# Kernel tuning notes

Hardware: AMD Instinct MI355X
Metric: run time of the kernel (lower is better)

The kernel has to match this reference:

```python
import jax, jax.numpy as jnp
import numpy as np

NEG_BIG = -9e15  # matches torch's -9000000000000000.0 mask value
LEAKY_SLOPE = 0.2  # alpha passed to nn.LeakyReLU


def setup_inputs() -> dict:
    key = jax.random.key(0)
    k1, k2, k3, k4, k5 = jax.random.split(key, 5)
    N, din, de, dout = 500, 100, 200, 100
    return {
        "input_relations": jax.random.normal(k1, (N, din), dtype=jnp.float32),
        "input_entity_embeds": jax.random.normal(k2, (N, N, de), dtype=jnp.float32),
        "relation_adj": jax.random.randint(k3, (N, N), 0, 2, dtype=jnp.int32),
        "a": jax.random.normal(k4, (dout, 2 * din + de), dtype=jnp.float32) * 0.05,
        "a_2": jax.random.normal(k5, (1, dout), dtype=jnp.float32) * 0.05,
    }


def reference(input_relations, input_entity_embeds, relation_adj, a, a_2):
    # Faithful to: a_input[k=(i,j)] = concat(rel_i, rel_j, ent[i,j]); e = a @ a_input
    # We avoid materializing the (N*N, 2*din+de) concat by splitting `a` into the
    # three blocks that hit rel_i, rel_j and ent[i,j] respectively.
    N, din = input_relations.shape
    de = input_entity_embeds.shape[-1]
    a_src = a[:, :din]          # (dout, din) acts on rel_i
    a_dst = a[:, din:2 * din]   # (dout, din) acts on rel_j
    a_ent = a[:, 2 * din:]      # (dout, de)  acts on ent[i,j]

    # e[i, j, o] = a @ concat(rel_i, rel_j, ent_ij)   -> (N, N, dout)
    e = (
        (input_relations @ a_src.T)[:, None, :]
        + (input_relations @ a_dst.T)[None, :, :]
        + jnp.einsum("ijd,od->ijo", input_entity_embeds.reshape(N, N, de), a_ent)
    )

    # scalar score per pair, leaky relu, masked softmax over neighbors j (dim=1)
    e2 = jax.nn.leaky_relu(e @ a_2[0], LEAKY_SLOPE)  # (N, N)
    scores = jnp.where(relation_adj > 0, e2, jnp.float32(NEG_BIG))
    attention = jax.nn.softmax(scores, axis=1)  # (N, N)

    # weighted sum of the score features e (note: original multiplies attention by e,
    # the pre-leakyrelu linear scores, not by a transformed h)
    h_prime = jnp.einsum("ij,ijo->io", attention, e)  # (N, dout)
    return jax.nn.elu(h_prime)  # concat=True branch
```

## Files before the change

kernel.cpp:

```cpp
#include <hip/hip_runtime.h>
#include <stdint.h>
#include <math.h>

#define N     500
#define DIN   100
#define DE    200
#define DOUT  100
#define AROW  (2*DIN + DE)
#define SLOPE 0.2f

#define JCH   8
#define CROWS 63
#define KP    512
#define BK    720
#define DEP   208

typedef __attribute__((ext_vector_type(8)))  short short8;
typedef __attribute__((ext_vector_type(16))) float f32x16;

static __device__ __forceinline__ unsigned short f2bf(float f) {
  union { float f; uint32_t u; } v; v.f = f;
  uint32_t r = (v.u + 0x7FFFu + ((v.u >> 16) & 1u)) >> 16;
  return (unsigned short)r;
}

__global__ __launch_bounds__(256)
void setup_kernel(const float* __restrict__ R, const float* __restrict__ A,
                  const float* __restrict__ a2,
                  float* __restrict__ src, float* __restrict__ ssrc,
                  float* __restrict__ sdst, float* __restrict__ wv,
                  unsigned short* __restrict__ Bcat, unsigned short* __restrict__ Pbuf) {
  int b = blockIdx.x, t = threadIdx.x;
  if (b < N) {
    int i = b;
    __shared__ float rrow[DIN];
    __shared__ float sred[4];
    if (t < DIN) rrow[t] = R[i * DIN + t];
    if (t < KP - N) Pbuf[i * KP + N + t] = 0;
    __syncthreads();
    int o = -1; bool isSrc = false;
    if (t < DOUT) { o = t; isSrc = true; }
    else if (t >= 128 && t < 128 + DOUT) { o = t - 128; }
    float val = 0.f;
    if (o >= 0) {
      const float* arow = A + o * AROW + (isSrc ? 0 : DIN);
      #pragma unroll 4
      for (int d = 0; d < DIN; ++d) val += rrow[d] * arow[d];
      if (isSrc) src[i * DOUT + o] = val;
      else       Bcat[o * BK + i] = f2bf(val);
    }
    float red = (o >= 0) ? val * a2[o] : 0.f;
    #pragma unroll
    for (int k = 1; k < 64; k <<= 1) red += __shfl_xor(red, k, 64);
    if ((t & 63) == 0) sred[t >> 6] = red;
    __syncthreads();
    if (t == 0)   ssrc[i] = sred[0] + sred[1];
    if (t == 128) sdst[i] = sred[2] + sred[3];
  } else if (b == N) {
    if (t < DE) {
      float s = 0.f;
      for (int o = 0; o < DOUT; ++o) s += A[o * AROW + 2 * DIN + t] * a2[o];
      wv[t] = s;
    }
  } else {
    int o = b - (N + 1);
    if (t < DE) Bcat[o * BK + KP + t] = f2bf(A[o * AROW + 2 * DIN + t]);
    if (t < KP - N) Bcat[o * BK + N + t] = 0;
    if (t >= 32 && t < 32 + (BK - KP - DE)) Bcat[o * BK + KP + DE + (t - 32)] = 0;
  }
}

__global__ __launch_bounds__(128)
void passA(const float* __restrict__ E, const int* __restrict__ adj,
           const float* __restrict__ ssrcA, const float* __restrict__ sdstA,
           const float* __restrict__ wv,
           unsigned short* __restrict__ Pbuf,
           float* __restrict__ gws, float* __restrict__ Zws) {
  int bid = blockIdx.x;
  int i = bid >> 3, c = bid & 7;
  int jbeg = c * CROWS;
  int jend = jbeg + CROWS; if (jend > N) jend = N;
  int t = threadIdx.x, wid = t >> 6, lane = t & 63;

  float4 w4 = make_float4(0.f, 0.f, 0.f, 0.f);
  if (lane < 50) w4 = *(const float4*)(wv + lane * 4);

  float4 g = make_float4(0.f, 0.f, 0.f, 0.f);
  float Z = 0.f;
  float ssrc_i = ssrcA[i];
  const float* Erow = E + (size_t)i * N * DE;
  const int* adjrow = adj + (size_t)i * N;

  int j = jbeg + wid;
  for (; j + 2 < jend; j += 4) {
    int a0 = adjrow[j], a1 = adjrow[j + 2];
    float4 ev0 = make_float4(0.f, 0.f, 0.f, 0.f);
    float4 ev1 = make_float4(0.f, 0.f, 0.f, 0.f);
    if (a0 > 0 && lane < 50) ev0 = *(const float4*)(Erow + (size_t)j * DE + lane * 4);
    if (a1 > 0 && lane < 50) ev1 = *(const float4*)(Erow + (size_t)(j + 2) * DE + lane * 4);
    float d0 = ev0.x * w4.x + ev0.y * w4.y + ev0.z * w4.z + ev0.w * w4.w;
    float d1 = ev1.x * w4.x + ev1.y * w4.y + ev1.z * w4.z + ev1.w * w4.w;
    #pragma unroll
    for (int k = 1; k < 64; k <<= 1) { d0 += __shfl_xor(d0, k, 64); d1 += __shfl_xor(d1, k, 64); }
    float p0 = 0.f, p1 = 0.f;
    if (a0 > 0) {
      float e2 = ssrc_i + sdstA[j] + d0;
      e2 = e2 > 0.f ? e2 : SLOPE * e2;
      p0 = __expf(e2); Z += p0;
      g.x += p0 * ev0.x; g.y += p0 * ev0.y; g.z += p0 * ev0.z; g.w += p0 * ev0.w;
    }
    if (a1 > 0) {
      float e2 = ssrc_i + sdstA[j + 2] + d1;
      e2 = e2 > 0.f ? e2 : SLOPE * e2;
      p1 = __expf(e2); Z += p1;
      g.x += p1 * ev1.x; g.y += p1 * ev1.y; g.z += p1 * ev1.z; g.w += p1 * ev1.w;
    }
    if (lane == 0) { Pbuf[i * KP + j] = f2bf(p0); Pbuf[i * KP + j + 2] = f2bf(p1); }
  }
  for (; j < jend; j += 2) {
    int a0 = adjrow[j];
    float4 ev0 = make_float4(0.f, 0.f, 0.f, 0.f);
    float p0 = 0.f;
    if (a0 > 0) {
      if (lane < 50) ev0 = *(const float4*)(Erow + (size_t)j * DE + lane * 4);
      float d0 = ev0.x * w4.x + ev0.y * w4.y + ev0.z * w4.z + ev0.w * w4.w;
      #pragma unroll
      for (int k = 1; k < 64; k <<= 1) d0 += __shfl_xor(d0, k, 64);
      float e2 = ssrc_i + sdstA[j] + d0;
      e2 = e2 > 0.f ? e2 : SLOPE * e2;
      p0 = __expf(e2); Z += p0;
      g.x += p0 * ev0.x; g.y += p0 * ev0.y; g.z += p0 * ev0.z; g.w += p0 * ev0.w;
    }
    if (lane == 0) Pbuf[i * KP + j] = f2bf(p0);
  }

  __shared__ float gl[2][200];
  __shared__ float zl[2];
  if (lane < 50) *(float4*)&gl[wid][lane * 4] = g;
  if (lane == 0) zl[wid] = Z;
  __syncthreads();
  if (wid == 0) {
    if (lane < 50) {
      float4 a = *(float4*)&gl[0][lane * 4];
      float4 b = *(float4*)&gl[1][lane * 4];
      *(float4*)(gws + (size_t)(i * JCH + c) * DE + lane * 4) =
          make_float4(a.x + b.x, a.y + b.y, a.z + b.z, a.w + b.w);
    }
    if (lane == 0) Zws[i * JCH + c] = zl[0] + zl[1];
  }
}

__global__ __launch_bounds__(64)
void gsum_kernel(const float* __restrict__ gws, const float* __restrict__ Zws,
                 unsigned short* __restrict__ gsum, float* __restrict__ Zsum) {
  int i = blockIdx.x, t = threadIdx.x;
  if (t < 50) {
    float4 s = make_float4(0.f, 0.f, 0.f, 0.f);
    #pragma unroll
    for (int c = 0; c < JCH; ++c) {
      float4 v = *(const float4*)(gws + (size_t)(i * JCH + c) * DE + t * 4);
      s.x += v.x; s.y += v.y; s.z += v.z; s.w += v.w;
    }
    ushort4 pk; pk.x = f2bf(s.x); pk.y = f2bf(s.y); pk.z = f2bf(s.z); pk.w = f2bf(s.w);
    *(ushort4*)(gsum + (size_t)i * DEP + t * 4) = pk;
  } else if (t == 50) {
    ushort4 z = {0, 0, 0, 0};
    *(ushort4*)(gsum + (size_t)i * DEP + 200) = z;
    *(ushort4*)(gsum + (size_t)i * DEP + 204) = z;
  } else if (t == 51) {
    float z = 0.f;
    #pragma unroll
    for (int c = 0; c < JCH; ++c) z += Zws[i * JCH + c];
    Zsum[i] = z;
  }
}

__global__ __launch_bounds__(256)
void combine_kernel(const float* __restrict__ src,
                    const unsigned short* __restrict__ Pbuf,
                    const unsigned short* __restrict__ Bcat,
                    const unsigned short* __restrict__ gsum,
                    const float* __restrict__ Zsum,
                    float* __restrict__ out) {
  int b = blockIdx.x;
  int t = threadIdx.x;
  int i0 = b * 32;
  int wave = t >> 6, lane = t & 63, c31 = lane & 31, hi = lane >> 5;
  int o = wave * 32 + c31;
  int arow = i0 + c31; if (arow > N - 1) arow = N - 1;

  const unsigned short* Prow = Pbuf + (size_t)arow * KP;
  const unsigned short* grow = gsum + (size_t)arow * DEP;

  f32x16 acc = {};
  #pragma unroll
  for (int ks = 0; ks < 45; ++ks) {
    short8 a, bf;
    if (ks < 32) a = *(const short8*)(Prow + ks * 16 + hi * 8);
    else         a = *(const short8*)(grow + (ks - 32) * 16 + hi * 8);
    if (o < DOUT) bf = *(const short8*)(Bcat + (size_t)o * BK + ks * 16 + hi * 8);
    else { short8 zz = {}; bf = zz; }
    acc = __builtin_amdgcn_mfma_f32_32x32x16_bf16(a, bf, acc, 0, 0, 0);
  }

  if (o < DOUT) {
    #pragma unroll
    for (int r = 0; r < 16; ++r) {
      int row = (r & 3) + 8 * (r >> 2) + 4 * hi;
      int i = i0 + row;
      if (i < N) {
        float h = src[i * DOUT + o] + acc[r] / Zsum[i];
        out[i * DOUT + o] = h > 0.f ? h : expm1f(h);
      }
    }
  }
}

extern "C" void kernel_launch(void* const* d_in, const int* in_sizes, int n_in,
                              void* d_out, int out_size, void* d_ws, size_t ws_size,
                              hipStream_t stream) {
  const float* R   = (const float*)d_in[0];
  const float* E   = (const float*)d_in[1];
  const int*   adj = (const int*)d_in[2];
  const float* A   = (const float*)d_in[3];
  const float* a2  = (const float*)d_in[4];
  float* out = (float*)d_out;

  char* wsb = (char*)d_ws;
  float*          src  = (float*)(wsb + 0);
  float*          ssrc = (float*)(wsb + 200000);
  float*          sdst = (float*)(wsb + 202000);
  float*          wv   = (float*)(wsb + 204000);
  unsigned short* Bcat = (unsigned short*)(wsb + 204800);
  unsigned short* Pbuf = (unsigned short*)(wsb + 348800);
  float*          gws  = (float*)(wsb + 860800);
  float*          Zws  = (float*)(wsb + 4060800);
  unsigned short* gsum = (unsigned short*)(wsb + 4076800);
  float*          Zsum = (float*)(wsb + 4284800);

  setup_kernel<<<N + 1 + DOUT, 256, 0, stream>>>(R, A, a2, src, ssrc, sdst, wv, Bcat, Pbuf);
  passA<<<N * JCH, 128, 0, stream>>>(E, adj, ssrc, sdst, wv, Pbuf, gws, Zws);
  gsum_kernel<<<N, 64, 0, stream>>>(gws, Zws, gsum, Zsum);
  combine_kernel<<<16, 256, 0, stream>>>(src, Pbuf, Bcat, gsum, Zsum, out);
}
```

Baseline: 64.38 us.

## Compact active neighbors per chunk and reduce partials with atomics, dropping gsum kernel

Measured after the change: 57.53 us. 10.6% less time.

```diff
diff --git a/kernel.cpp b/kernel.cpp
--- a/kernel.cpp
+++ b/kernel.cpp
@@ -9,11 +9,12 @@
 #define AROW  (2*DIN + DE)
 #define SLOPE 0.2f
 
-#define JCH   8
-#define CROWS 63
+#define JCH   4
+#define CROWS 125
 #define KP    512
 #define BK    720
 #define DEP   208
+#define GZF   104000
 
 typedef __attribute__((ext_vector_type(8)))  short short8;
 typedef __attribute__((ext_vector_type(16))) float f32x16;
@@ -29,7 +30,8 @@
                   const float* __restrict__ a2,
                   float* __restrict__ src, float* __restrict__ ssrc,
                   float* __restrict__ sdst, float* __restrict__ wv,
-                  unsigned short* __restrict__ Bcat, unsigned short* __restrict__ Pbuf) {
+                  unsigned short* __restrict__ Bcat, unsigned short* __restrict__ Pbuf,
+                  float* __restrict__ gsum, float* __restrict__ Zsum) {
   int b = blockIdx.x, t = threadIdx.x;
   if (b < N) {
     int i = b;
@@ -62,124 +64,121 @@
       for (int o = 0; o < DOUT; ++o) s += A[o * AROW + 2 * DIN + t] * a2[o];
       wv[t] = s;
     }
-  } else {
+  } else if (b <= N + DOUT) {
     int o = b - (N + 1);
     if (t < DE) Bcat[o * BK + KP + t] = f2bf(A[o * AROW + 2 * DIN + t]);
     if (t < KP - N) Bcat[o * BK + N + t] = 0;
     if (t >= 32 && t < 32 + (BK - KP - DE)) Bcat[o * BK + KP + DE + (t - 32)] = 0;
-  }
-}
-
-__global__ __launch_bounds__(128)
+  } else if (b <= 702) {
+    int off = (b - 601) * 1024 + t * 4;
+    if (off < GZF) *(float4*)(gsum + off) = make_float4(0.f, 0.f, 0.f, 0.f);
+  } else {
+    if (t < 125) *(float4*)(Zsum + t * 4) = make_float4(0.f, 0.f, 0.f, 0.f);
+  }
+}
+
+__global__ __launch_bounds__(256)
 void passA(const float* __restrict__ E, const int* __restrict__ adj,
            const float* __restrict__ ssrcA, const float* __restrict__ sdstA,
            const float* __restrict__ wv,
            unsigned short* __restrict__ Pbuf,
-           float* __restrict__ gws, float* __restrict__ Zws) {
+           float* __restrict__ gsum, float* __restrict__ Zsum) {
+  __shared__ int list[128];
+  __shared__ int cntS;
+  __shared__ float gl[4][200];
+  __shared__ float zl[4];
+
   int bid = blockIdx.x;
-  int i = bid >> 3, c = bid & 7;
+  int i = bid >> 2, c = bid & 3;
   int jbeg = c * CROWS;
-  int jend = jbeg + CROWS; if (jend > N) jend = N;
   int t = threadIdx.x, wid = t >> 6, lane = t & 63;
+
+  if (t == 0) cntS = 0;
+  __syncthreads();
+
+  bool active = false;
+  if (t < CROWS) active = (adj[(size_t)i * N + jbeg + t] > 0);
+  unsigned long long mask = __ballot(active);
+  int wbase = 0;
+  if (lane == 0 && mask) wbase = atomicAdd(&cntS, __popcll(mask));
+  wbase = __shfl(wbase, 0);
+  if (active) {
+    list[wbase + __popcll(mask & ((1ull << lane) - 1ull))] = jbeg + t;
+  } else if (t < CROWS) {
+    Pbuf[i * KP + jbeg + t] = 0;
+  }
+  __syncthreads();
+  int cnt = cntS;
 
   float4 w4 = make_float4(0.f, 0.f, 0.f, 0.f);
   if (lane < 50) w4 = *(const float4*)(wv + lane * 4);
-
   float4 g = make_float4(0.f, 0.f, 0.f, 0.f);
   float Z = 0.f;
   float ssrc_i = ssrcA[i];
   const float* Erow = E + (size_t)i * N * DE;
-  const int* adjrow = adj + (size_t)i * N;
-
-  int j = jbeg + wid;
-  for (; j + 2 < jend; j += 4) {
-    int a0 = adjrow[j], a1 = adjrow[j + 2];
-    float4 ev0 = make_float4(0.f, 0.f, 0.f, 0.f);
-    float4 ev1 = make_float4(0.f, 0.f, 0.f, 0.f);
-    if (a0 > 0 && lane < 50) ev0 = *(const float4*)(Erow + (size_t)j * DE + lane * 4);
-    if (a1 > 0 && lane < 50) ev1 = *(const float4*)(Erow + (size_t)(j + 2) * DE + lane * 4);
-    float d0 = ev0.x * w4.x + ev0.y * w4.y + ev0.z * w4.z + ev0.w * w4.w;
-    float d1 = ev1.x * w4.x + ev1.y * w4.y + ev1.z * w4.z + ev1.w * w4.w;
-    #pragma unroll
-    for (int k = 1; k < 64; k <<= 1) { d0 += __shfl_xor(d0, k, 64); d1 += __shfl_xor(d1, k, 64); }
-    float p0 = 0.f, p1 = 0.f;
-    if (a0 > 0) {
-      float e2 = ssrc_i + sdstA[j] + d0;
-      e2 = e2 > 0.f ? e2 : SLOPE * e2;
-      p0 = __expf(e2); Z += p0;
-      g.x += p0 * ev0.x; g.y += p0 * ev0.y; g.z += p0 * ev0.z; g.w += p0 * ev0.w;
-    }
-    if (a1 > 0) {
-      float e2 = ssrc_i + sdstA[j + 2] + d1;
-      e2 = e2 > 0.f ? e2 : SLOPE * e2;
-      p1 = __expf(e2); Z += p1;
-      g.x += p1 * ev1.x; g.y += p1 * ev1.y; g.z += p1 * ev1.z; g.w += p1 * ev1.w;
-    }
-    if (lane == 0) { Pbuf[i * KP + j] = f2bf(p0); Pbuf[i * KP + j + 2] = f2bf(p1); }
-  }
-  for (; j < jend; j += 2) {
-    int a0 = adjrow[j];
-    float4 ev0 = make_float4(0.f, 0.f, 0.f, 0.f);
-    float p0 = 0.f;
-    if (a0 > 0) {
-      if (lane < 50) ev0 = *(const float4*)(Erow + (size_t)j * DE + lane * 4);
-      float d0 = ev0.x * w4.x + ev0.y * w4.y + ev0.z * w4.z + ev0.w * w4.w;
-      #pragma unroll
-      for (int k = 1; k < 64; k <<= 1) d0 += __shfl_xor(d0, k, 64);
-      float e2 = ssrc_i + sdstA[j] + d0;
-      e2 = e2 > 0.f ? e2 : SLOPE * e2;
-      p0 = __expf(e2); Z += p0;
-      g.x += p0 * ev0.x; g.y += p0 * ev0.y; g.z += p0 * ev0.z; g.w += p0 * ev0.w;
-    }
-    if (lane == 0) Pbuf[i * KP + j] = f2bf(p0);
-  }
-
-  __shared__ float gl[2][200];
-  __shared__ float zl[2];
+
+  for (int base = wid * 4; base + 3 < cnt; base += 16) {
+    int j0 = list[base], j1 = list[base + 1], j2 = list[base + 2], j3 = list[base + 3];
+    float4 e0 = make_float4(0.f,0.f,0.f,0.f), e1 = e0, e2v = e0, e3 = e0;
+    if (lane < 50) {
+      e0  = *(const float4*)(Erow + (size_t)j0 * DE + lane * 4);
+      e1  = *(const float4*)(Erow + (size_t)j1 * DE + lane * 4);
+      e2v = *(const float4*)(Erow + (size_t)j2 * DE + lane * 4);
+      e3  = *(const float4*)(Erow + (size_t)j3 * DE + lane * 4);
+    }
+    float d0 = e0.x*w4.x + e0.y*w4.y + e0.z*w4.z + e0.w*w4.w;
+    float d1 = e1.x*w4.x + e1.y*w4.y + e1.z*w4.z + e1.w*w4.w;
+    float d2 = e2v.x*w4.x + e2v.y*w4.y + e2v.z*w4.z + e2v.w*w4.w;
+    float d3 = e3.x*w4.x + e3.y*w4.y + e3.z*w4.z + e3.w*w4.w;
+    #pragma unroll
+    for (int k = 1; k < 64; k <<= 1) {
+      d0 += __shfl_xor(d0, k); d1 += __shfl_xor(d1, k);
+      d2 += __shfl_xor(d2, k); d3 += __shfl_xor(d3, k);
+    }
+    float s0 = ssrc_i + sdstA[j0] + d0; s0 = s0 > 0.f ? s0 : SLOPE * s0;
+    float s1 = ssrc_i + sdstA[j1] + d1; s1 = s1 > 0.f ? s1 : SLOPE * s1;
+    float s2 = ssrc_i + sdstA[j2] + d2; s2 = s2 > 0.f ? s2 : SLOPE * s2;
+    float s3 = ssrc_i + sdstA[j3] + d3; s3 = s3 > 0.f ? s3 : SLOPE * s3;
+    float p0 = __expf(s0), p1 = __expf(s1), p2 = __expf(s2), p3 = __expf(s3);
+    Z += (p0 + p1) + (p2 + p3);
+    g.x += p0*e0.x + p1*e1.x + p2*e2v.x + p3*e3.x;
+    g.y += p0*e0.y + p1*e1.y + p2*e2v.y + p3*e3.y;
+    g.z += p0*e0.z + p1*e1.z + p2*e2v.z + p3*e3.z;
+    g.w += p0*e0.w + p1*e1.w + p2*e2v.w + p3*e3.w;
+    if (lane == 0) {
+      Pbuf[i * KP + j0] = f2bf(p0); Pbuf[i * KP + j1] = f2bf(p1);
+      Pbuf[i * KP + j2] = f2bf(p2); Pbuf[i * KP + j3] = f2bf(p3);
+    }
+  }
+  for (int idx = (cnt & ~3) + wid; idx < cnt; idx += 4) {
+    int j = list[idx];
+    float4 ev = make_float4(0.f,0.f,0.f,0.f);
+    if (lane < 50) ev = *(const float4*)(Erow + (size_t)j * DE + lane * 4);
+    float d = ev.x*w4.x + ev.y*w4.y + ev.z*w4.z + ev.w*w4.w;
+    #pragma unroll
+    for (int k = 1; k < 64; k <<= 1) d += __shfl_xor(d, k);
+    float s = ssrc_i + sdstA[j] + d; s = s > 0.f ? s : SLOPE * s;
+    float p = __expf(s);
+    Z += p;
+    g.x += p*ev.x; g.y += p*ev.y; g.z += p*ev.z; g.w += p*ev.w;
+    if (lane == 0) Pbuf[i * KP + j] = f2bf(p);
+  }
+
   if (lane < 50) *(float4*)&gl[wid][lane * 4] = g;
   if (lane == 0) zl[wid] = Z;
   __syncthreads();
-  if (wid == 0) {
-    if (lane < 50) {
-      float4 a = *(float4*)&gl[0][lane * 4];
-      float4 b = *(float4*)&gl[1][lane * 4];
-      *(float4*)(gws + (size_t)(i * JCH + c) * DE + lane * 4) =
-          make_float4(a.x + b.x, a.y + b.y, a.z + b.z, a.w + b.w);
-    }
-    if (lane == 0) Zws[i * JCH + c] = zl[0] + zl[1];
-  }
-}
-
-__global__ __launch_bounds__(64)
-void gsum_kernel(const float* __restrict__ gws, const float* __restrict__ Zws,
-                 unsigned short* __restrict__ gsum, float* __restrict__ Zsum) {
-  int i = blockIdx.x, t = threadIdx.x;
-  if (t < 50) {
-    float4 s = make_float4(0.f, 0.f, 0.f, 0.f);
-    #pragma unroll
-    for (int c = 0; c < JCH; ++c) {
-      float4 v = *(const float4*)(gws + (size_t)(i * JCH + c) * DE + t * 4);
-      s.x += v.x; s.y += v.y; s.z += v.z; s.w += v.w;
-    }
-    ushort4 pk; pk.x = f2bf(s.x); pk.y = f2bf(s.y); pk.z = f2bf(s.z); pk.w = f2bf(s.w);
-    *(ushort4*)(gsum + (size_t)i * DEP + t * 4) = pk;
-  } else if (t == 50) {
-    ushort4 z = {0, 0, 0, 0};
-    *(ushort4*)(gsum + (size_t)i * DEP + 200) = z;
-    *(ushort4*)(gsum + (size_t)i * DEP + 204) = z;
-  } else if (t == 51) {
-    float z = 0.f;
-    #pragma unroll
-    for (int c = 0; c < JCH; ++c) z += Zws[i * JCH + c];
-    Zsum[i] = z;
-  }
+  if (t < 200) {
+    float s = gl[0][t] + gl[1][t] + gl[2][t] + gl[3][t];
+    atomicAdd(gsum + (size_t)i * DEP + t, s);
+  }
+  if (t == 200) atomicAdd(Zsum + i, zl[0] + zl[1] + zl[2] + zl[3]);
 }
 
 __global__ __launch_bounds__(256)
 void combine_kernel(const float* __restrict__ src,
                     const unsigned short* __restrict__ Pbuf,
                     const unsigned short* __restrict__ Bcat,
-                    const unsigned short* __restrict__ gsum,
+                    const float* __restrict__ gsum,
                     const float* __restrict__ Zsum,
                     float* __restrict__ out) {
   int b = blockIdx.x;
@@ -190,14 +189,23 @@
   int arow = i0 + c31; if (arow > N - 1) arow = N - 1;
 
   const unsigned short* Prow = Pbuf + (size_t)arow * KP;
-  const unsigned short* grow = gsum + (size_t)arow * DEP;
+  const float* grow = gsum + (size_t)arow * DEP;
 
   f32x16 acc = {};
   #pragma unroll
   for (int ks = 0; ks < 45; ++ks) {
     short8 a, bf;
-    if (ks < 32) a = *(const short8*)(Prow + ks * 16 + hi * 8);
-    else         a = *(const short8*)(grow + (ks - 32) * 16 + hi * 8);
+    if (ks < 32) {
+      a = *(const short8*)(Prow + ks * 16 + hi * 8);
+    } else {
+      int d0 = (ks - 32) * 16 + hi * 8;
+      float4 ga = *(const float4*)(grow + d0);
+      float4 gb = *(const float4*)(grow + d0 + 4);
+      a[0] = (short)f2bf(ga.x); a[1] = (short)f2bf(ga.y);
+      a[2] = (short)f2bf(ga.z); a[3] = (short)f2bf(ga.w);
+      a[4] = (short)f2bf(gb.x); a[5] = (short)f2bf(gb.y);
+      a[6] = (short)f2bf(gb.z); a[7] = (short)f2bf(gb.w);
+    }
     if (o < DOUT) bf = *(const short8*)(Bcat + (size_t)o * BK + ks * 16 + hi * 8);
     else { short8 zz = {}; bf = zz; }
     acc = __builtin_amdgcn_mfma_f32_32x32x16_bf16(a, bf, acc, 0, 0, 0);
@@ -233,13 +241,10 @@
   float*          wv   = (float*)(wsb + 204000);
   unsigned short* Bcat = (unsigned short*)(wsb + 204800);
   unsigned short* Pbuf = (unsigned short*)(wsb + 348800);
-  float*          gws  = (float*)(wsb + 860800);
-  float*          Zws  = (float*)(wsb + 4060800);
-  unsigned short* gsum = (unsigned short*)(wsb + 4076800);
-  float*          Zsum = (float*)(wsb + 4284800);
-
-  setup_kernel<<<N + 1 + DOUT, 256, 0, stream>>>(R, A, a2, src, ssrc, sdst, wv, Bcat, Pbuf);
-  passA<<<N * JCH, 128, 0, stream>>>(E, adj, ssrc, sdst, wv, Pbuf, gws, Zws);
-  gsum_kernel<<<N, 64, 0, stream>>>(gws, Zws, gsum, Zsum);
+  float*          gsum = (float*)(wsb + 860800);
+  float*          Zsum = (float*)(wsb + 1276800);
+
+  setup_kernel<<<704, 256, 0, stream>>>(R, A, a2, src, ssrc, sdst, wv, Bcat, Pbuf, gsum, Zsum);
+  passA<<<N * JCH, 256, 0, stream>>>(E, adj, ssrc, sdst, wv, Pbuf, gsum, Zsum);
   combine_kernel<<<16, 256, 0, stream>>>(src, Pbuf, Bcat, gsum, Zsum, out);
 }
```
